# Kernel optimization log

Hardware: AMD Instinct MI355X
Metric: run time of the kernel (lower is better)

Reference implementation:

```python
import jax, jax.numpy as jnp
import numpy as np

N_NODES = 50000
N_EDGES = 800000
NFEAT, NHID, NCLASS = 512, 128, 40
BN_EPS = 1e-5


def setup_inputs() -> dict:
    key = jax.random.key(0)
    ks = jax.random.split(key, 12)
    x = jax.random.normal(ks[0], (N_NODES, NFEAT), dtype=jnp.float32)
    edge_index = jax.random.randint(ks[1], (2, N_EDGES), 0, N_NODES, dtype=jnp.int64)
    edge_weight = jax.random.uniform(ks[2], (N_EDGES,), dtype=jnp.float32)
    def glorot(k, fi, fo):
        lim = (6.0 / (fi + fo)) ** 0.5
        return jax.random.uniform(k, (fi, fo), minval=-lim, maxval=lim, dtype=jnp.float32)
    return {
        "x": x, "edge_index": edge_index, "edge_weight": edge_weight,
        "W1": glorot(ks[3], NFEAT, NHID), "b1": jnp.zeros((NHID,), jnp.float32),
        "W2": glorot(ks[4], NHID, NHID), "b2": jnp.zeros((NHID,), jnp.float32),
        "W3": glorot(ks[5], NHID, NHID), "b3": jnp.zeros((NHID,), jnp.float32),
        "g1": jnp.ones((NHID,), jnp.float32), "be1": jnp.zeros((NHID,), jnp.float32),
        "g2": jnp.ones((NHID,), jnp.float32), "be2": jnp.zeros((NHID,), jnp.float32),
        "g3": jnp.ones((NHID,), jnp.float32), "be3": jnp.zeros((NHID,), jnp.float32),
        "linW": glorot(ks[6], NHID, NCLASS), "linb": jnp.zeros((NCLASS,), jnp.float32),
    }


def _gcn_norm(edge_index, edge_weight, n):
    # PyG gcn_norm: add self-loops (weight 1), symmetric D^-1/2 (A+I) D^-1/2
    loop = jnp.arange(n, dtype=edge_index.dtype)
    row = jnp.concatenate([edge_index[0], loop])
    col = jnp.concatenate([edge_index[1], loop])
    ew = jnp.concatenate([edge_weight, jnp.ones((n,), edge_weight.dtype)])
    deg = jax.ops.segment_sum(ew, col, num_segments=n)
    dinv = jnp.where(deg > 0, jax.lax.rsqrt(jnp.maximum(deg, 1e-30)), 0.0)
    norm = dinv[row] * ew * dinv[col]
    return row, col, norm


def _conv(x, W, b, row, col, norm, n):
    h = x @ W                                   # [N, out]
    msg = h[row] * norm[:, None]                # gather + weight, [E+N, out]
    return jax.ops.segment_sum(msg, col, num_segments=n) + b


def _bn(x, g, b):
    # training-mode BatchNorm over node dim (biased variance)
    mu = jnp.mean(x, axis=0)
    var = jnp.mean((x - mu) ** 2, axis=0)
    return (x - mu) * jax.lax.rsqrt(var + BN_EPS) * g + b


def reference(x, edge_index, edge_weight, W1, b1, W2, b2, W3, b3,
              g1, be1, g2, be2, g3, be3, linW, linb):
    n = x.shape[0]
    row, col, norm = _gcn_norm(edge_index, edge_weight, n)
    x1 = _bn(jax.nn.relu(_conv(x, W1, b1, row, col, norm, n)), g1, be1)
    x2 = _bn(jax.nn.relu(_conv(x1, W2, b2, row, col, norm, n)), g2, be2)
    x3 = _bn(_conv(x2, W3, b3, row, col, norm, n), g3, be3)
    logits = x3 @ linW + linb
    return (logits, jax.nn.softmax(logits, axis=1), x3)
```

## Files before the change

kernel.cpp:

```cpp
#include <hip/hip_runtime.h>
#include <hip/hip_bf16.h>

#define N_NODES 50000
#define N_EDGES 800000
#define NFEAT 512
#define NHID 128
#define NCLASS 40
#define BN_EPS 1e-5f

typedef __attribute__((ext_vector_type(8))) short short8;
typedef __attribute__((ext_vector_type(4))) float f32x4;

#define GEMM1_BLOCKS ((N_NODES + 127) / 128)
#define GEMMH_BLOCKS ((N_NODES + 127) / 128)
#define EDGE_BLOCKS ((N_EDGES + 255) / 256)
#define SCAN_BLOCKS ((N_NODES + 255) / 256)
#define BN_BLOCKS ((N_NODES + 255) / 256)
#define AGG_BLOCKS ((N_NODES * 64 + 255) / 256)

__device__ __forceinline__ unsigned short f2b(float f) {
    unsigned int u = __float_as_uint(f);
    u += 0x7fff + ((u >> 16) & 1);
    return (unsigned short)(u >> 16);
}
__device__ __forceinline__ unsigned int pk2(float lo, float hi) {
    unsigned int r;
    asm("v_cvt_pk_bf16_f32 %0, %1, %2" : "=v"(r) : "v"(lo), "v"(hi));
    return r;
}
__device__ __forceinline__ float blo(unsigned int v) {
    return __uint_as_float(v << 16);
}
__device__ __forceinline__ float bhi(unsigned int v) {
    return __uint_as_float(v & 0xffff0000u);
}

__global__ void k_prep_w(const float* __restrict__ W1, const float* __restrict__ W2,
                         const float* __restrict__ W3, unsigned short* __restrict__ W1t,
                         unsigned short* __restrict__ W2t, unsigned short* __restrict__ W3t,
                         unsigned long long* __restrict__ degcnt,
                         float* __restrict__ stats, int* __restrict__ syncp) {
    int i = blockIdx.x * blockDim.x + threadIdx.x;
    if (i < N_NODES) degcnt[i] = 0ULL;
    if (i < 768) stats[i] = 0.f;
    else if (i < 776) syncp[i - 768] = 0;
    if (i < 65536) {
        int k = i >> 7, n = i & 127;
        W1t[n * 512 + k] = f2b(W1[i]);
    } else if (i < 81920) {
        int j = i - 65536; int k = j >> 7, n = j & 127;
        W2t[n * 128 + k] = f2b(W2[j]);
    } else if (i < 98304) {
        int j = i - 81920; int k = j >> 7, n = j & 127;
        W3t[n * 128 + k] = f2b(W3[j]);
    }
}

__global__ __launch_bounds__(256) void k_edges(
    const unsigned int* __restrict__ words, const float* __restrict__ ew,
    int* __restrict__ row, int* __restrict__ col,
    unsigned long long* __restrict__ degcnt, int* __restrict__ slot) {
    __shared__ int s_any;
    int tid = threadIdx.x;
    if (tid == 0) s_any = 0;
    __syncthreads();
    unsigned int probe = words[2 * tid + 1];
    if (probe != 0) atomicAdd(&s_any, 1);
    __syncthreads();
    int f = (s_any == 0) ? 1 : 0;
    int e = blockIdx.x * 256 + tid;
    if (e < N_EDGES) {
        unsigned int r = f ? words[2 * (size_t)e] : words[e];
        unsigned int c = f ? words[2 * ((size_t)e + N_EDGES)] : words[e + N_EDGES];
        row[e] = (int)r;
        col[e] = (int)c;
        unsigned int q = __float2uint_rn(ew[e] * 8388608.0f);
        unsigned long long old = atomicAdd(&degcnt[c], (1ULL << 32) | (unsigned long long)q);
        slot[e] = (int)(old >> 32);
    }
}

__global__ __launch_bounds__(256) void k_gemm1(
    const float* __restrict__ x, const unsigned short* __restrict__ W1t,
    unsigned short* __restrict__ hbuf) {
    __shared__ unsigned short As[128][40];
    __shared__ unsigned short Bs[128][40];
    int tid = threadIdx.x;
    int m0 = blockIdx.x * 128;
    int srow = tid >> 1;
    int skh = (tid & 1) << 4;
    int wave = tid >> 6, lane = tid & 63;
    int wm = (wave >> 1) * 64, wn = (wave & 1) * 64;
    int l15 = lane & 15, quad = lane >> 4;
    f32x4 acc[4][4] = {};
    bool arow_ok = (m0 + srow) < N_NODES;
    const float* arow_p = x + (size_t)(m0 + srow) * 512 + skh;
    const unsigned short* wrow_p = W1t + (size_t)srow * 512 + skh;
    float4 ta[4];
    uint4 tb0, tb1;
#pragma unroll
    for (int q = 0; q < 4; q++) {
        ta[q] = make_float4(0.f, 0.f, 0.f, 0.f);
        if (arow_ok) ta[q] = *(const float4*)(arow_p + q * 4);
    }
    tb0 = *(const uint4*)(wrow_p);
    tb1 = *(const uint4*)(wrow_p + 8);
    for (int kt = 0; kt < 512; kt += 32) {
        unsigned int p[8];
#pragma unroll
        for (int q = 0; q < 4; q++) {
            p[2 * q]     = pk2(ta[q].x, ta[q].y);
            p[2 * q + 1] = pk2(ta[q].z, ta[q].w);
        }
        *(uint4*)&As[srow][skh] = make_uint4(p[0], p[1], p[2], p[3]);
        *(uint4*)&As[srow][skh + 8] = make_uint4(p[4], p[5], p[6], p[7]);
        *(uint4*)&Bs[srow][skh] = tb0;
        *(uint4*)&Bs[srow][skh + 8] = tb1;
        __syncthreads();
        if (kt + 32 < 512) {
#pragma unroll
            for (int q = 0; q < 4; q++) {
                float4 t4 = make_float4(0.f, 0.f, 0.f, 0.f);
                if (arow_ok) t4 = *(const float4*)(arow_p + kt + 32 + q * 4);
                ta[q] = t4;
            }
            tb0 = *(const uint4*)(wrow_p + kt + 32);
            tb1 = *(const uint4*)(wrow_p + kt + 40);
        }
        short8 a[4], b[4];
#pragma unroll
        for (int i = 0; i < 4; i++) a[i] = *(const short8*)&As[wm + i * 16 + l15][quad * 8];
#pragma unroll
        for (int j = 0; j < 4; j++) b[j] = *(const short8*)&Bs[wn + j * 16 + l15][quad * 8];
#pragma unroll
        for (int i = 0; i < 4; i++)
#pragma unroll
            for (int j = 0; j < 4; j++)
                acc[i][j] = __builtin_amdgcn_mfma_f32_16x16x32_bf16(a[i], b[j], acc[i][j], 0, 0, 0);
        __syncthreads();
    }
#pragma unroll
    for (int i = 0; i < 4; i++) {
        int mb = m0 + wm + i * 16 + quad * 4;
#pragma unroll
        for (int r = 0; r < 4; r++) {
            int m = mb + r;
            if (m < N_NODES) {
#pragma unroll
                for (int j = 0; j < 4; j++)
                    hbuf[(size_t)m * 128 + wn + j * 16 + l15] = f2b(acc[i][j][r]);
            }
        }
    }
}

__global__ __launch_bounds__(256) void k_dinv(const unsigned long long* __restrict__ degcnt,
                                              float* __restrict__ dinv,
                                              int* __restrict__ counts,
                                              int* __restrict__ bsum,
                                              int* __restrict__ ticket,
                                              int* __restrict__ bpre,
                                              int* __restrict__ colptr) {
    int i = blockIdx.x * 256 + threadIdx.x;
    int cnt = 0;
    if (i < N_NODES) {
        unsigned long long v = degcnt[i];
        float deg = 1.0f + (float)(unsigned int)(v & 0xffffffffULL) * (1.0f / 8388608.0f);
        dinv[i] = rsqrtf(deg);
        cnt = (int)(v >> 32);
        counts[i] = cnt;
    }
    __shared__ int sh[256];
    __shared__ int s_last;
    sh[threadIdx.x] = cnt;
    __syncthreads();
    for (int ofs = 128; ofs > 0; ofs >>= 1) {
        if (threadIdx.x < ofs) sh[threadIdx.x] += sh[threadIdx.x + ofs];
        __syncthreads();
    }
    if (threadIdx.x == 0) {
        bsum[blockIdx.x] = sh[0];
        __threadfence();
        int t = atomicAdd(ticket, 1);
        s_last = (t == SCAN_BLOCKS - 1) ? 1 : 0;
    }
    __syncthreads();
    if (s_last) {
        __threadfence();
        int t = threadIdx.x;
        int v = (t < SCAN_BLOCKS) ? ((volatile int*)bsum)[t] : 0;
        sh[t] = v;
        __syncthreads();
        for (int ofs = 1; ofs < 256; ofs <<= 1) {
            int u = (t >= ofs) ? sh[t - ofs] : 0;
            __syncthreads();
            sh[t] += u;
            __syncthreads();
        }
        if (t < SCAN_BLOCKS) bpre[t] = sh[t] - v;
        if (t == SCAN_BLOCKS - 1) colptr[N_NODES] = sh[t];
    }
}

__global__ __launch_bounds__(256) void k_scan3(const int* __restrict__ counts,
                                               const int* __restrict__ bpre,
                                               int* __restrict__ colptr) {
    int t = threadIdx.x;
    int i = blockIdx.x * 256 + t;
    int v = (i < N_NODES) ? counts[i] : 0;
    __shared__ int sh[256];
    sh[t] = v;
    __syncthreads();
    for (int ofs = 1; ofs < 256; ofs <<= 1) {
        int u = (t >= ofs) ? sh[t - ofs] : 0;
        __syncthreads();
        sh[t] += u;
        __syncthreads();
    }
    if (i < N_NODES) colptr[i] = bpre[blockIdx.x] + sh[t] - v;
}

__global__ void k_scatter(const int* __restrict__ row, const int* __restrict__ col,
                          const float* __restrict__ ew, const float* __restrict__ dinv,
                          const int* __restrict__ colptr, const int* __restrict__ slot,
                          int2* __restrict__ ern) {
    int e = blockIdx.x * blockDim.x + threadIdx.x;
    if (e < N_EDGES) {
        int c = col[e], r = row[e];
        int p = colptr[c] + slot[e];
        float nrm = dinv[r] * ew[e] * dinv[c];
        ern[p] = make_int2(r, __float_as_int(nrm));
    }
}

__global__ __launch_bounds__(256) void k_aggregate(
    const unsigned int* __restrict__ hb, const int* __restrict__ colptr,
    const int2* __restrict__ ern, const float* __restrict__ dinv,
    const float* __restrict__ bias, unsigned int* __restrict__ out, int relu) {
    int node = (blockIdx.x * blockDim.x + threadIdx.x) >> 6;
    int lane = threadIdx.x & 63;
    if (node >= N_NODES) return;
    float di = dinv[node];
    float selfw = di * di;
    unsigned int sv = hb[(size_t)node * 64 + lane];
    float a0 = selfw * blo(sv);
    float a1 = selfw * bhi(sv);
    float c0 = 0.f, c1 = 0.f;
    int start = colptr[node], end = colptr[node + 1];
    int nfull = (end - start) & ~7;
    if (nfull) {
        int e = start;
        int2 rwc[8];
#pragma unroll
        for (int q = 0; q < 8; q++) rwc[q] = ern[e + q];
        for (;;) {
            int en = e + 8;
            bool more = (en < start + nfull);
            int2 rwn[8];
            if (more) {
#pragma unroll
                for (int q = 0; q < 8; q++) rwn[q] = ern[en + q];
            }
            unsigned int v[8];
#pragma unroll
            for (int q = 0; q < 8; q++) v[q] = hb[(size_t)rwc[q].x * 64 + lane];
#pragma unroll
            for (int q = 0; q < 8; q++) {
                float w = __int_as_float(rwc[q].y);
                if (q & 1) { c0 += w * blo(v[q]); c1 += w * bhi(v[q]); }
                else       { a0 += w * blo(v[q]); a1 += w * bhi(v[q]); }
            }
            if (!more) break;
#pragma unroll
            for (int q = 0; q < 8; q++) rwc[q] = rwn[q];
            e = en;
        }
    }
    for (int e = start + nfull; e < end; e++) {
        int2 rw = ern[e];
        float w = __int_as_float(rw.y);
        unsigned int v = hb[(size_t)rw.x * 64 + lane];
        a0 += w * blo(v);
        a1 += w * bhi(v);
    }
    a0 += c0; a1 += c1;
    float2 bv = *(const float2*)&bias[2 * lane];
    a0 += bv.x;
    a1 += bv.y;
    if (relu) { a0 = fmaxf(a0, 0.f); a1 = fmaxf(a1, 0.f); }
    out[(size_t)node * 64 + lane] = pk2(a0, a1);
}

__global__ __launch_bounds__(256) void k_bnstats(const unsigned int* __restrict__ x,
                                                 float* __restrict__ sums,
                                                 float* __restrict__ sumsq) {
    int u = threadIdx.x & 63;
    int strip = threadIdx.x >> 6;
    int r0 = blockIdx.x * 256;
    int rend = min(r0 + 256, N_NODES);
    float sl = 0.f, s2l = 0.f, sh_ = 0.f, s2h = 0.f;
    for (int r = r0 + strip; r < rend; r += 4) {
        unsigned int v = x[(size_t)r * 64 + u];
        float a = blo(v), b = bhi(v);
        sl += a; s2l += a * a;
        sh_ += b; s2h += b * b;
    }
    __shared__ float buf[4][64][4];
    buf[strip][u][0] = sl; buf[strip][u][1] = s2l;
    buf[strip][u][2] = sh_; buf[strip][u][3] = s2h;
    __syncthreads();
    if (strip == 0) {
#pragma unroll
        for (int s = 1; s < 4; s++) {
            sl += buf[s][u][0]; s2l += buf[s][u][1];
            sh_ += buf[s][u][2]; s2h += buf[s][u][3];
        }
        atomicAdd(&sums[2 * u], sl);
        atomicAdd(&sums[2 * u + 1], sh_);
        atomicAdd(&sumsq[2 * u], s2l);
        atomicAdd(&sumsq[2 * u + 1], s2h);
    }
}

__global__ __launch_bounds__(256) void k_gemm_h(
    const unsigned int* __restrict__ Ab, const unsigned short* __restrict__ Wt,
    const float* __restrict__ sums, const float* __restrict__ sumsq,
    const float* __restrict__ g, const float* __restrict__ be,
    unsigned short* __restrict__ Out) {
    __shared__ unsigned short As[128][40];
    __shared__ unsigned short Bs[128][40];
    __shared__ float s_sc[128], s_sh[128];
    int tid = threadIdx.x;
    int m0 = blockIdx.x * 128;
    if (tid < 128) {
        const float invn = 1.0f / (float)N_NODES;
        float mu = sums[tid] * invn;
        float var = sumsq[tid] * invn - mu * mu;
        float iv = rsqrtf(var + BN_EPS);
        float sc = g[tid] * iv;
        s_sc[tid] = sc;
        s_sh[tid] = be[tid] - mu * sc;
    }
    __syncthreads();
    int srow = tid >> 1;
    int skh = (tid & 1) << 4;
    int wave = tid >> 6, lane = tid & 63;
    int wm = (wave >> 1) * 64, wn = (wave & 1) * 64;
    int l15 = lane & 15, quad = lane >> 4;
    f32x4 acc[4][4] = {};
    bool arow_ok = (m0 + srow) < N_NODES;
    const unsigned int* arow_b = Ab + (size_t)(m0 + srow) * 64 + (skh >> 1);
    const unsigned short* wrow_p = Wt + (size_t)srow * 128 + skh;
    uint4 r0 = make_uint4(0, 0, 0, 0), r1 = make_uint4(0, 0, 0, 0);
    uint4 tb0, tb1;
    if (arow_ok) {
        r0 = *(const uint4*)(arow_b);
        r1 = *(const uint4*)(arow_b + 4);
    }
    tb0 = *(const uint4*)(wrow_p);
    tb1 = *(const uint4*)(wrow_p + 8);
    for (int kt = 0; kt < 128; kt += 32) {
        unsigned int raw[8] = {r0.x, r0.y, r0.z, r0.w, r1.x, r1.y, r1.z, r1.w};
        unsigned int p[8];
#pragma unroll
        for (int q = 0; q < 8; q++) {
            int ch = kt + skh + 2 * q;
            float f0 = blo(raw[q]) * s_sc[ch] + s_sh[ch];
            float f1 = bhi(raw[q]) * s_sc[ch + 1] + s_sh[ch + 1];
            p[q] = pk2(f0, f1);
        }
        *(uint4*)&As[srow][skh] = make_uint4(p[0], p[1], p[2], p[3]);
        *(uint4*)&As[srow][skh + 8] = make_uint4(p[4], p[5], p[6], p[7]);
        *(uint4*)&Bs[srow][skh] = tb0;
        *(uint4*)&Bs[srow][skh + 8] = tb1;
        __syncthreads();
        if (kt + 32 < 128) {
            if (arow_ok) {
                r0 = *(const uint4*)(arow_b + ((kt + 32) >> 1));
                r1 = *(const uint4*)(arow_b + ((kt + 32) >> 1) + 4);
            }
            tb0 = *(const uint4*)(wrow_p + kt + 32);
            tb1 = *(const uint4*)(wrow_p + kt + 40);
        }
        short8 a[4], b[4];
#pragma unroll
        for (int i = 0; i < 4; i++) a[i] = *(const short8*)&As[wm + i * 16 + l15][quad * 8];
#pragma unroll
        for (int j = 0; j < 4; j++) b[j] = *(const short8*)&Bs[wn + j * 16 + l15][quad * 8];
#pragma unroll
        for (int i = 0; i < 4; i++)
#pragma unroll
            for (int j = 0; j < 4; j++)
                acc[i][j] = __builtin_amdgcn_mfma_f32_16x16x32_bf16(a[i], b[j], acc[i][j], 0, 0, 0);
        __syncthreads();
    }
#pragma unroll
    for (int i = 0; i < 4; i++) {
        int mb = m0 + wm + i * 16 + quad * 4;
#pragma unroll
        for (int r = 0; r < 4; r++) {
            int m = mb + r;
            if (m < N_NODES) {
#pragma unroll
                for (int j = 0; j < 4; j++)
                    Out[(size_t)m * 128 + wn + j * 16 + l15] = f2b(acc[i][j][r]);
            }
        }
    }
}

__global__ __launch_bounds__(256) void k_logits(const unsigned int* __restrict__ abuf,
                                                const float* __restrict__ sums,
                                                const float* __restrict__ sumsq,
                                                const float* __restrict__ g,
                                                const float* __restrict__ be,
                                                const float* __restrict__ linW,
                                                const float* __restrict__ linb,
                                                float* __restrict__ logits,
                                                float* __restrict__ probs,
                                                float* __restrict__ x3out) {
    __shared__ float Xs[64][130];
    __shared__ float Ws[128 * 40];
    __shared__ float s_sc[128], s_sh[128];
    int tid = threadIdx.x;
    int m0 = blockIdx.x * 64;
    if (tid < 128) {
        const float invn = 1.0f / (float)N_NODES;
        float mu = sums[tid] * invn;
        float var = sumsq[tid] * invn - mu * mu;
        float iv = rsqrtf(var + BN_EPS);
        float sc = g[tid] * iv;
        s_sc[tid] = sc;
        s_sh[tid] = be[tid] - mu * sc;
    }
    for (int q = tid; q < 1280; q += 256)
        *(float4*)&Ws[q * 4] = *(const float4*)&linW[q * 4];
    __syncthreads();
    for (int q = tid; q < 4096; q += 256) {
        int r = q >> 6, u = q & 63;
        int m = m0 + r;
        float f0 = 0.f, f1 = 0.f;
        if (m < N_NODES) {
            unsigned int v = abuf[(size_t)m * 64 + u];
            f0 = blo(v) * s_sc[2 * u] + s_sh[2 * u];
            f1 = bhi(v) * s_sc[2 * u + 1] + s_sh[2 * u + 1];
            *(float2*)&x3out[(size_t)m * 128 + 2 * u] = make_float2(f0, f1);
        }
        *(float2*)&Xs[r][2 * u] = make_float2(f0, f1);
    }
    __syncthreads();
    int r = tid >> 2;
    int cg = tid & 3;
    int cbase = cg * 10;
    float acc[10] = {};
    for (int k = 0; k < 128; k++) {
        float a = Xs[r][k];
#pragma unroll
        for (int j = 0; j < 10; j++) acc[j] += a * Ws[k * 40 + cbase + j];
    }
#pragma unroll
    for (int j = 0; j < 10; j++) acc[j] += linb[cbase + j];
    float m = acc[0];
#pragma unroll
    for (int j = 1; j < 10; j++) m = fmaxf(m, acc[j]);
    m = fmaxf(m, __shfl_xor(m, 1));
    m = fmaxf(m, __shfl_xor(m, 2));
    float ex[10];
    float s = 0.f;
#pragma unroll
    for (int j = 0; j < 10; j++) { ex[j] = expf(acc[j] - m); s += ex[j]; }
    s += __shfl_xor(s, 1);
    s += __shfl_xor(s, 2);
    float inv = 1.0f / s;
    int mrow = m0 + r;
    if (mrow < N_NODES) {
#pragma unroll
        for (int j = 0; j < 10; j += 2) {
            *(float2*)&logits[(size_t)mrow * 40 + cbase + j] = make_float2(acc[j], acc[j + 1]);
            *(float2*)&probs[(size_t)mrow * 40 + cbase + j] = make_float2(ex[j] * inv, ex[j + 1] * inv);
        }
    }
}

extern "C" void kernel_launch(void* const* d_in, const int* in_sizes, int n_in,
                              void* d_out, int out_size, void* d_ws, size_t ws_size,
                              hipStream_t stream) {
    const float* x = (const float*)d_in[0];
    const unsigned int* eidx = (const unsigned int*)d_in[1];
    const float* ew = (const float*)d_in[2];
    const float* W1 = (const float*)d_in[3];
    const float* b1 = (const float*)d_in[4];
    const float* W2 = (const float*)d_in[5];
    const float* b2 = (const float*)d_in[6];
    const float* W3 = (const float*)d_in[7];
    const float* b3 = (const float*)d_in[8];
    const float* g1 = (const float*)d_in[9];
    const float* be1 = (const float*)d_in[10];
    const float* g2 = (const float*)d_in[11];
    const float* be2 = (const float*)d_in[12];
    const float* g3 = (const float*)d_in[13];
    const float* be3 = (const float*)d_in[14];
    const float* linW = (const float*)d_in[15];
    const float* linb = (const float*)d_in[16];

    float* out = (float*)d_out;
    float* logits = out;
    float* probs = out + (size_t)N_NODES * NCLASS;
    float* x3out = out + 2 * (size_t)N_NODES * NCLASS;

    char* ws = (char*)d_ws;
    size_t off = 0;
    auto take = [&](size_t bytes) -> char* {
        char* p = ws + off;
        off += (bytes + 255) & ~(size_t)255;
        return p;
    };
    int* row32 = (int*)take((size_t)N_EDGES * 4);
    int* col32 = (int*)take((size_t)N_EDGES * 4);
    int* slot = (int*)take((size_t)N_EDGES * 4);
    int* colptr = (int*)take((size_t)(N_NODES + 1) * 4);
    int* counts = (int*)take((size_t)N_NODES * 4);
    unsigned long long* degcnt = (unsigned long long*)take((size_t)N_NODES * 8);
    int2* ern = (int2*)take((size_t)N_EDGES * 8);
    float* dinv = (float*)take((size_t)N_NODES * 4);
    unsigned short* hbuf = (unsigned short*)take((size_t)N_NODES * NHID * 2);
    unsigned short* abuf = (unsigned short*)take((size_t)N_NODES * NHID * 2);
    unsigned short* W1t = (unsigned short*)take((size_t)512 * 128 * 2);
    unsigned short* W2t = (unsigned short*)take((size_t)128 * 128 * 2);
    unsigned short* W3t = (unsigned short*)take((size_t)128 * 128 * 2);
    float* stats = (float*)take(768 * 4);
    int* syncp = (int*)take(8 * 4);
    int* bsum = (int*)take((size_t)SCAN_BLOCKS * 4);
    int* bpre = (int*)take((size_t)SCAN_BLOCKS * 4);
    (void)ws_size; (void)n_in; (void)in_sizes; (void)out_size;

    float* sums1 = stats, *sumsq1 = stats + 128;
    float* sums2 = stats + 256, *sumsq2 = stats + 384;
    float* sums3 = stats + 512, *sumsq3 = stats + 640;

    const int TPB = 256;

    k_prep_w<<<(98304 + TPB - 1) / TPB, TPB, 0, stream>>>(W1, W2, W3, W1t, W2t, W3t, degcnt, stats, syncp);
    k_edges<<<EDGE_BLOCKS, TPB, 0, stream>>>(eidx, ew, row32, col32, degcnt, slot);
    k_gemm1<<<GEMM1_BLOCKS, TPB, 0, stream>>>(x, W1t, hbuf);
    k_dinv<<<SCAN_BLOCKS, TPB, 0, stream>>>(degcnt, dinv, counts, bsum, &syncp[0], bpre, colptr);
    k_scan3<<<SCAN_BLOCKS, TPB, 0, stream>>>(counts, bpre, colptr);
    k_scatter<<<EDGE_BLOCKS, TPB, 0, stream>>>(row32, col32, ew, dinv, colptr, slot, ern);

    k_aggregate<<<AGG_BLOCKS, TPB, 0, stream>>>((const unsigned int*)hbuf, colptr, ern, dinv, b1, (unsigned int*)abuf, 1);
    k_bnstats<<<BN_BLOCKS, TPB, 0, stream>>>((const unsigned int*)abuf, sums1, sumsq1);

    k_gemm_h<<<GEMMH_BLOCKS, TPB, 0, stream>>>((const unsigned int*)abuf, W2t, sums1, sumsq1, g1, be1, hbuf);
    k_aggregate<<<AGG_BLOCKS, TPB, 0, stream>>>((const unsigned int*)hbuf, colptr, ern, dinv, b2, (unsigned int*)abuf, 1);
    k_bnstats<<<BN_BLOCKS, TPB, 0, stream>>>((const unsigned int*)abuf, sums2, sumsq2);

    k_gemm_h<<<GEMMH_BLOCKS, TPB, 0, stream>>>((const unsigned int*)abuf, W3t, sums2, sumsq2, g2, be2, hbuf);
    k_aggregate<<<AGG_BLOCKS, TPB, 0, stream>>>((const unsigned int*)hbuf, colptr, ern, dinv, b3, (unsigned int*)abuf, 0);
    k_bnstats<<<BN_BLOCKS, TPB, 0, stream>>>((const unsigned int*)abuf, sums3, sumsq3);

    k_logits<<<(N_NODES + 63) / 64, TPB, 0, stream>>>((const unsigned int*)abuf, sums3, sumsq3, g3, be3, linW, linb, logits, probs, x3out);
}
```

Before: 547.1 us.

## Fuse edge preprocessing with first GEMM, simplify aggregation loop, unroll BN stats

Merges the edge-parsing/degree-count kernel and the first feature GEMM into one launch with block-index dispatch, so the two independent stages can run concurrently and one launch is saved. The aggregation inner loop drops the software-pipelined full-chunk loop plus scalar tail in favour of a single predicated 8-wide loop that masks out-of-range edges with zero weight. The BatchNorm statistics loop now issues four loads per iteration to increase memory-level parallelism. Costs include wasted masked gathers for low-degree nodes, the loss of prefetching of edge records, and the GEMM's shared-memory footprint now also being allocated for the edge blocks.

Measured after the change: 452.2 us. 1.21x faster.

```diff
diff --git a/kernel.cpp b/kernel.cpp
--- a/kernel.cpp
+++ b/kernel.cpp
@@ -56,100 +56,99 @@
     }
 }
 
-__global__ __launch_bounds__(256) void k_edges(
+__global__ __launch_bounds__(256) void k_fat(
+    const float* __restrict__ x, const unsigned short* __restrict__ W1t,
+    unsigned short* __restrict__ hbuf,
     const unsigned int* __restrict__ words, const float* __restrict__ ew,
     int* __restrict__ row, int* __restrict__ col,
     unsigned long long* __restrict__ degcnt, int* __restrict__ slot) {
+    __shared__ unsigned short As[128][40];
+    __shared__ unsigned short Bs[128][40];
     __shared__ int s_any;
     int tid = threadIdx.x;
-    if (tid == 0) s_any = 0;
-    __syncthreads();
-    unsigned int probe = words[2 * tid + 1];
-    if (probe != 0) atomicAdd(&s_any, 1);
-    __syncthreads();
-    int f = (s_any == 0) ? 1 : 0;
-    int e = blockIdx.x * 256 + tid;
-    if (e < N_EDGES) {
-        unsigned int r = f ? words[2 * (size_t)e] : words[e];
-        unsigned int c = f ? words[2 * ((size_t)e + N_EDGES)] : words[e + N_EDGES];
-        row[e] = (int)r;
-        col[e] = (int)c;
-        unsigned int q = __float2uint_rn(ew[e] * 8388608.0f);
-        unsigned long long old = atomicAdd(&degcnt[c], (1ULL << 32) | (unsigned long long)q);
-        slot[e] = (int)(old >> 32);
-    }
-}
-
-__global__ __launch_bounds__(256) void k_gemm1(
-    const float* __restrict__ x, const unsigned short* __restrict__ W1t,
-    unsigned short* __restrict__ hbuf) {
-    __shared__ unsigned short As[128][40];
-    __shared__ unsigned short Bs[128][40];
-    int tid = threadIdx.x;
-    int m0 = blockIdx.x * 128;
-    int srow = tid >> 1;
-    int skh = (tid & 1) << 4;
-    int wave = tid >> 6, lane = tid & 63;
-    int wm = (wave >> 1) * 64, wn = (wave & 1) * 64;
-    int l15 = lane & 15, quad = lane >> 4;
-    f32x4 acc[4][4] = {};
-    bool arow_ok = (m0 + srow) < N_NODES;
-    const float* arow_p = x + (size_t)(m0 + srow) * 512 + skh;
-    const unsigned short* wrow_p = W1t + (size_t)srow * 512 + skh;
-    float4 ta[4];
-    uint4 tb0, tb1;
-#pragma unroll
-    for (int q = 0; q < 4; q++) {
-        ta[q] = make_float4(0.f, 0.f, 0.f, 0.f);
-        if (arow_ok) ta[q] = *(const float4*)(arow_p + q * 4);
-    }
-    tb0 = *(const uint4*)(wrow_p);
-    tb1 = *(const uint4*)(wrow_p + 8);
-    for (int kt = 0; kt < 512; kt += 32) {
-        unsigned int p[8];
+    if (blockIdx.x < GEMM1_BLOCKS) {
+        int m0 = blockIdx.x * 128;
+        int srow = tid >> 1;
+        int skh = (tid & 1) << 4;
+        int wave = tid >> 6, lane = tid & 63;
+        int wm = (wave >> 1) * 64, wn = (wave & 1) * 64;
+        int l15 = lane & 15, quad = lane >> 4;
+        f32x4 acc[4][4] = {};
+        bool arow_ok = (m0 + srow) < N_NODES;
+        const float* arow_p = x + (size_t)(m0 + srow) * 512 + skh;
+        const unsigned short* wrow_p = W1t + (size_t)srow * 512 + skh;
+        float4 ta[4];
+        uint4 tb0, tb1;
 #pragma unroll
         for (int q = 0; q < 4; q++) {
-            p[2 * q]     = pk2(ta[q].x, ta[q].y);
-            p[2 * q + 1] = pk2(ta[q].z, ta[q].w);
-        }
-        *(uint4*)&As[srow][skh] = make_uint4(p[0], p[1], p[2], p[3]);
-        *(uint4*)&As[srow][skh + 8] = make_uint4(p[4], p[5], p[6], p[7]);
-        *(uint4*)&Bs[srow][skh] = tb0;
-        *(uint4*)&Bs[srow][skh + 8] = tb1;
-        __syncthreads();
-        if (kt + 32 < 512) {
+            ta[q] = make_float4(0.f, 0.f, 0.f, 0.f);
+            if (arow_ok) ta[q] = *(const float4*)(arow_p + q * 4);
+        }
+        tb0 = *(const uint4*)(wrow_p);
+        tb1 = *(const uint4*)(wrow_p + 8);
+        for (int kt = 0; kt < 512; kt += 32) {
+            unsigned int p[8];
 #pragma unroll
             for (int q = 0; q < 4; q++) {
-                float4 t4 = make_float4(0.f, 0.f, 0.f, 0.f);
-                if (arow_ok) t4 = *(const float4*)(arow_p + kt + 32 + q * 4);
-                ta[q] = t4;
+                p[2 * q]     = pk2(ta[q].x, ta[q].y);
+                p[2 * q + 1] = pk2(ta[q].z, ta[q].w);
             }
-            tb0 = *(const uint4*)(wrow_p + kt + 32);
-            tb1 = *(const uint4*)(wrow_p + kt + 40);
-        }
-        short8 a[4], b[4];
-#pragma unroll
-        for (int i = 0; i < 4; i++) a[i] = *(const short8*)&As[wm + i * 16 + l15][quad * 8];
-#pragma unroll
-        for (int j = 0; j < 4; j++) b[j] = *(const short8*)&Bs[wn + j * 16 + l15][quad * 8];
-#pragma unroll
-        for (int i = 0; i < 4; i++)
-#pragma unroll
-            for (int j = 0; j < 4; j++)
-                acc[i][j] = __builtin_amdgcn_mfma_f32_16x16x32_bf16(a[i], b[j], acc[i][j], 0, 0, 0);
-        __syncthreads();
-    }
-#pragma unroll
-    for (int i = 0; i < 4; i++) {
-        int mb = m0 + wm + i * 16 + quad * 4;
-#pragma unroll
-        for (int r = 0; r < 4; r++) {
-            int m = mb + r;
-            if (m < N_NODES) {
+            *(uint4*)&As[srow][skh] = make_uint4(p[0], p[1], p[2], p[3]);
+            *(uint4*)&As[srow][skh + 8] = make_uint4(p[4], p[5], p[6], p[7]);
+            *(uint4*)&Bs[srow][skh] = tb0;
+            *(uint4*)&Bs[srow][skh + 8] = tb1;
+            __syncthreads();
+            if (kt + 32 < 512) {
+#pragma unroll
+                for (int q = 0; q < 4; q++) {
+                    float4 t4 = make_float4(0.f, 0.f, 0.f, 0.f);
+                    if (arow_ok) t4 = *(const float4*)(arow_p + kt + 32 + q * 4);
+                    ta[q] = t4;
+                }
+                tb0 = *(const uint4*)(wrow_p + kt + 32);
+                tb1 = *(const uint4*)(wrow_p + kt + 40);
+            }
+            short8 a[4], b[4];
+#pragma unroll
+            for (int i = 0; i < 4; i++) a[i] = *(const short8*)&As[wm + i * 16 + l15][quad * 8];
+#pragma unroll
+            for (int j = 0; j < 4; j++) b[j] = *(const short8*)&Bs[wn + j * 16 + l15][quad * 8];
+#pragma unroll
+            for (int i = 0; i < 4; i++)
 #pragma unroll
                 for (int j = 0; j < 4; j++)
-                    hbuf[(size_t)m * 128 + wn + j * 16 + l15] = f2b(acc[i][j][r]);
+                    acc[i][j] = __builtin_amdgcn_mfma_f32_16x16x32_bf16(a[i], b[j], acc[i][j], 0, 0, 0);
+            __syncthreads();
+        }
+#pragma unroll
+        for (int i = 0; i < 4; i++) {
+            int mb = m0 + wm + i * 16 + quad * 4;
+#pragma unroll
+            for (int r = 0; r < 4; r++) {
+                int m = mb + r;
+                if (m < N_NODES) {
+#pragma unroll
+                    for (int j = 0; j < 4; j++)
+                        hbuf[(size_t)m * 128 + wn + j * 16 + l15] = f2b(acc[i][j][r]);
+                }
             }
+        }
+    } else {
+        if (tid == 0) s_any = 0;
+        __syncthreads();
+        unsigned int probe = words[2 * tid + 1];
+        if (probe != 0) atomicAdd(&s_any, 1);
+        __syncthreads();
+        int f = (s_any == 0) ? 1 : 0;
+        int e = (blockIdx.x - GEMM1_BLOCKS) * 256 + tid;
+        if (e < N_EDGES) {
+            unsigned int r = f ? words[2 * (size_t)e] : words[e];
+            unsigned int c = f ? words[2 * ((size_t)e + N_EDGES)] : words[e + N_EDGES];
+            row[e] = (int)r;
+            col[e] = (int)c;
+            unsigned int q = __float2uint_rn(ew[e] * 8388608.0f);
+            unsigned long long old = atomicAdd(&degcnt[c], (1ULL << 32) | (unsigned long long)q);
+            slot[e] = (int)(old >> 32);
         }
     }
 }
@@ -247,41 +246,24 @@
     float a1 = selfw * bhi(sv);
     float c0 = 0.f, c1 = 0.f;
     int start = colptr[node], end = colptr[node + 1];
-    int nfull = (end - start) & ~7;
-    if (nfull) {
-        int e = start;
-        int2 rwc[8];
-#pragma unroll
-        for (int q = 0; q < 8; q++) rwc[q] = ern[e + q];
-        for (;;) {
-            int en = e + 8;
-            bool more = (en < start + nfull);
-            int2 rwn[8];
-            if (more) {
-#pragma unroll
-                for (int q = 0; q < 8; q++) rwn[q] = ern[en + q];
-            }
-            unsigned int v[8];
-#pragma unroll
-            for (int q = 0; q < 8; q++) v[q] = hb[(size_t)rwc[q].x * 64 + lane];
-#pragma unroll
-            for (int q = 0; q < 8; q++) {
-                float w = __int_as_float(rwc[q].y);
-                if (q & 1) { c0 += w * blo(v[q]); c1 += w * bhi(v[q]); }
-                else       { a0 += w * blo(v[q]); a1 += w * bhi(v[q]); }
-            }
-            if (!more) break;
-#pragma unroll
-            for (int q = 0; q < 8; q++) rwc[q] = rwn[q];
-            e = en;
-        }
-    }
-    for (int e = start + nfull; e < end; e++) {
-        int2 rw = ern[e];
-        float w = __int_as_float(rw.y);
-        unsigned int v = hb[(size_t)rw.x * 64 + lane];
-        a0 += w * blo(v);
-        a1 += w * bhi(v);
+    for (int e0 = start; e0 < end; e0 += 8) {
+        int2 rw[8];
+        float wq[8];
+#pragma unroll
+        for (int q = 0; q < 8; q++) {
+            int ee = e0 + q;
+            bool ok = ee < end;
+            rw[q] = ern[ok ? ee : start];
+            wq[q] = ok ? __int_as_float(rw[q].y) : 0.f;
+        }
+        unsigned int v[8];
+#pragma unroll
+        for (int q = 0; q < 8; q++) v[q] = hb[(size_t)rw[q].x * 64 + lane];
+#pragma unroll
+        for (int q = 0; q < 8; q++) {
+            if (q & 1) { c0 += wq[q] * blo(v[q]); c1 += wq[q] * bhi(v[q]); }
+            else       { a0 += wq[q] * blo(v[q]); a1 += wq[q] * bhi(v[q]); }
+        }
     }
     a0 += c0; a1 += c1;
     float2 bv = *(const float2*)&bias[2 * lane];
@@ -299,11 +281,19 @@
     int r0 = blockIdx.x * 256;
     int rend = min(r0 + 256, N_NODES);
     float sl = 0.f, s2l = 0.f, sh_ = 0.f, s2h = 0.f;
-    for (int r = r0 + strip; r < rend; r += 4) {
-        unsigned int v = x[(size_t)r * 64 + u];
-        float a = blo(v), b = bhi(v);
-        sl += a; s2l += a * a;
-        sh_ += b; s2h += b * b;
+    for (int r = r0 + strip; r < rend; r += 16) {
+        unsigned int v[4];
+#pragma unroll
+        for (int k = 0; k < 4; k++) {
+            int rr = r + 4 * k;
+            v[k] = (rr < rend) ? x[(size_t)rr * 64 + u] : 0u;
+        }
+#pragma unroll
+        for (int k = 0; k < 4; k++) {
+            float a = blo(v[k]), b = bhi(v[k]);
+            sl += a; s2l += a * a;
+            sh_ += b; s2h += b * b;
+        }
     }
     __shared__ float buf[4][64][4];
     buf[strip][u][0] = sl; buf[strip][u][1] = s2l;
@@ -541,8 +531,8 @@
     const int TPB = 256;
 
     k_prep_w<<<(98304 + TPB - 1) / TPB, TPB, 0, stream>>>(W1, W2, W3, W1t, W2t, W3t, degcnt, stats, syncp);
-    k_edges<<<EDGE_BLOCKS, TPB, 0, stream>>>(eidx, ew, row32, col32, degcnt, slot);
-    k_gemm1<<<GEMM1_BLOCKS, TPB, 0, stream>>>(x, W1t, hbuf);
+    k_fat<<<GEMM1_BLOCKS + EDGE_BLOCKS, TPB, 0, stream>>>(
+        x, W1t, hbuf, eidx, ew, row32, col32, degcnt, slot);
     k_dinv<<<SCAN_BLOCKS, TPB, 0, stream>>>(degcnt, dinv, counts, bsum, &syncp[0], bpre, colptr);
     k_scan3<<<SCAN_BLOCKS, TPB, 0, stream>>>(counts, bpre, colptr);
     k_scatter<<<EDGE_BLOCKS, TPB, 0, stream>>>(row32, col32, ew, dinv, colptr, slot, ern);
```
